# Optimization experiments

Hardware: AMD Instinct MI355X
Metric: run time of the kernel (lower is better)

Reference implementation:

```python
import jax, jax.numpy as jnp
import numpy as np

N_SPK, N_UTT, D_EMB = 1024, 20, 512
COS_EPS = 1e-8   # torch F.cosine_similarity default eps
SIM_EPS = 1e-6   # added to cosine and inside the log, per original code


def setup_inputs() -> dict:
    key = jax.random.key(0)
    embeddings = jax.random.normal(key, (N_SPK, N_UTT, D_EMB), dtype=jnp.float32)
    w = jnp.asarray(10.0, dtype=jnp.float32)
    b = jnp.asarray(-5.0, dtype=jnp.float32)
    return {"embeddings": embeddings, "w": w, "b": b}


def reference(embeddings, w, b):
    N, M, D = embeddings.shape
    sums = embeddings.sum(axis=1)                       # [N, D]
    centroids = sums / M                                # [N, D] full centroids
    cent_excl = (sums[:, None, :] - embeddings) / (M - 1)  # [N, M, D] leave-one-out

    def _norm(x):
        return x / jnp.maximum(jnp.linalg.norm(x, axis=-1, keepdims=True), COS_EPS)

    e_n = _norm(embeddings)          # [N, M, D]
    c_n = _norm(centroids)           # [N, D]
    ce_n = _norm(cent_excl)          # [N, M, D]

    # cosine vs every speaker centroid
    cs = jnp.einsum('nmd,kd->nmk', e_n, c_n)            # [N, M, N]
    # replace same-speaker column with leave-one-out cosine
    diag = jnp.sum(e_n * ce_n, axis=-1)                 # [N, M]
    same = jnp.eye(N, dtype=bool)[:, None, :]           # [N, 1, N]
    cossim = jnp.where(same, diag[:, :, None], cs) + SIM_EPS

    sim = w * cossim + b                                # [N, M, N]
    pos = w * (diag + SIM_EPS) + b                      # sim[j, i, j]
    lse = jnp.log(jnp.sum(jnp.exp(sim), axis=-1) + SIM_EPS)  # [N, M]
    loss = jnp.sum(lse - pos)
    return loss
```

## Files before the change

### kernel.cpp

```cpp
#include <hip/hip_runtime.h>
#include <hip/hip_bf16.h>

typedef unsigned short u16;
typedef unsigned int u32;
typedef __bf16 bf16x8 __attribute__((ext_vector_type(8)));
typedef float f32x4 __attribute__((ext_vector_type(4)));

#define NSPK 1024
#define NUTT 20
#define DEMB 512
#define NROW (NSPK * NUTT)

__device__ __forceinline__ u16 f2bf(float x) {
    union { float f; u32 u; } v; v.f = x;
    u32 r = (v.u + 0x7fffu + ((v.u >> 16) & 1u)) >> 16;
    return (u16)r;
}

__global__ __launch_bounds__(256) void sums_k(const float* __restrict__ E,
                                              float* __restrict__ S,
                                              u16* __restrict__ Bc,
                                              float* __restrict__ ssg,
                                              float* __restrict__ rs,
                                              float* __restrict__ out) {
    __shared__ float s_red[4];
    const int n = blockIdx.x;
    const int t = threadIdx.x;
    const int lane = t & 63, wv = t >> 6;
    const int d0 = t * 2;
    const float* En = E + (size_t)n * (NUTT * DEMB);

    float sx = 0.f, sy = 0.f;
#pragma unroll
    for (int m = 0; m < NUTT; ++m) {
        float2 v = *(const float2*)(En + m * DEMB + d0);
        sx += v.x; sy += v.y;
    }
    *(float2*)(S + (size_t)n * DEMB + d0) = make_float2(sx, sy);

    const float c0 = sx * (1.0f / NUTT), c1 = sy * (1.0f / NUTT);
    float p = c0 * c0 + c1 * c1;
#pragma unroll
    for (int o = 32; o; o >>= 1) p += __shfl_xor(p, o);
    if (lane == 0) s_red[wv] = p;
    __syncthreads();
    p = s_red[0] + s_red[1] + s_red[2] + s_red[3];
    const float rc = 1.0f / fmaxf(sqrtf(p), 1e-8f);
    const u16 cb0 = f2bf(c0 * rc), cb1 = f2bf(c1 * rc);
    *(u32*)(Bc + (size_t)n * DEMB + d0) = (u32)cb0 | ((u32)cb1 << 16);

    if (t == 0) {
        ssg[2 * n + 0] = p * (float)(NUTT * NUTT);
        ssg[2 * n + 1] = rc * (1.0f / NUTT);
    }
    if (t < NUTT) rs[n * NUTT + t] = 0.f;
    if (n == 0 && t == 0) out[0] = 0.f;
}

__global__ __launch_bounds__(256) void rowprep_k(const float* __restrict__ E,
                                                 const float* __restrict__ S,
                                                 const float* __restrict__ ssg,
                                                 u16* __restrict__ A,
                                                 float* __restrict__ diag,
                                                 float* __restrict__ csd) {
    const int lane = threadIdx.x & 63;
    const int r = blockIdx.x * 4 + (threadIdx.x >> 6);
    const int n = r / NUTT;

    const float* e = E + (size_t)r * DEMB + lane * 8;
    const float* s = S + (size_t)n * DEMB + lane * 8;
    const float4 e0 = *(const float4*)(e), e1 = *(const float4*)(e + 4);
    const float4 s0 = *(const float4*)(s), s1 = *(const float4*)(s + 4);

    float ee = e0.x*e0.x + e0.y*e0.y + e0.z*e0.z + e0.w*e0.w
             + e1.x*e1.x + e1.y*e1.y + e1.z*e1.z + e1.w*e1.w;
    float es = e0.x*s0.x + e0.y*s0.y + e0.z*s0.z + e0.w*s0.w
             + e1.x*s1.x + e1.y*s1.y + e1.z*s1.z + e1.w*s1.w;
#pragma unroll
    for (int o = 32; o; o >>= 1) { ee += __shfl_xor(ee, o); es += __shfl_xor(es, o); }

    const float ss = ssg[2 * n + 0], g = ssg[2 * n + 1];
    const float rne = 1.0f / fmaxf(sqrtf(ee), 1e-8f);
    const float pxx = ss - 2.f * es + ee;
    const float dg = (es - ee) * rne / fmaxf(sqrtf(pxx), 1.9e-7f);

    union { u16 h[8]; uint4 q; } pk;
    pk.h[0] = f2bf(e0.x * rne); pk.h[1] = f2bf(e0.y * rne);
    pk.h[2] = f2bf(e0.z * rne); pk.h[3] = f2bf(e0.w * rne);
    pk.h[4] = f2bf(e1.x * rne); pk.h[5] = f2bf(e1.y * rne);
    pk.h[6] = f2bf(e1.z * rne); pk.h[7] = f2bf(e1.w * rne);
    ((uint4*)(A + (size_t)r * DEMB))[lane] = pk.q;

    if (lane == 0) {
        diag[r] = dg;
        csd[r] = es * g * rne;
    }
}

__device__ __forceinline__ void async_copy16(const void* g, void* l) {
    __builtin_amdgcn_global_load_lds(
        (const __attribute__((address_space(1))) void*)g,
        (__attribute__((address_space(3))) void*)l, 16, 0, 0);
}

__global__ __launch_bounds__(256) void gemm_exp(const u16* __restrict__ A,
                                                const u16* __restrict__ Bc,
                                                const float* __restrict__ wp,
                                                const float* __restrict__ bp,
                                                float* __restrict__ rowsum) {
    __shared__ u16 As[128 * 32];
    __shared__ u16 Bs[128 * 32];
    const int t = threadIdx.x;
    const int lane = t & 63, wv = t >> 6;
    const int ml = lane & 15, q = lane >> 4;
    const int wm = wv >> 1, wn = wv & 1;
    const int tileM = blockIdx.x;
    const int tileN = blockIdx.y;

    const float w = *wp, bb = *bp;

    const int c0 = t, c1 = t + 256;
    const int r0 = c0 >> 2, kg0 = (c0 & 3) ^ ((r0 >> 1) & 3);
    const int r1 = c1 >> 2, kg1 = (c1 & 3) ^ ((r1 >> 1) & 3);
    const u16* Ag = A + (size_t)tileM * 128 * DEMB;
    const u16* Bg = Bc + (size_t)tileN * 128 * DEMB;
    u16* as0 = As + c0 * 8; u16* as1 = As + c1 * 8;
    u16* bs0 = Bs + c0 * 8; u16* bs1 = Bs + c1 * 8;

    int ar[4], br[4];
#pragma unroll
    for (int i = 0; i < 4; ++i) {
        int r = wm * 64 + i * 16 + ml;
        ar[i] = r * 32 + ((q ^ ((r >> 1) & 3)) << 3);
        int c = wn * 64 + i * 16 + ml;
        br[i] = c * 32 + ((q ^ ((c >> 1) & 3)) << 3);
    }

    f32x4 acc[4][4];
#pragma unroll
    for (int i = 0; i < 4; ++i)
#pragma unroll
        for (int j = 0; j < 4; ++j) acc[i][j] = (f32x4){0.f, 0.f, 0.f, 0.f};

    for (int kt = 0; kt < DEMB; kt += 32) {
        __syncthreads();
        async_copy16(Ag + (size_t)r0 * DEMB + kt + kg0 * 8, as0);
        async_copy16(Ag + (size_t)r1 * DEMB + kt + kg1 * 8, as1);
        async_copy16(Bg + (size_t)r0 * DEMB + kt + kg0 * 8, bs0);
        async_copy16(Bg + (size_t)r1 * DEMB + kt + kg1 * 8, bs1);
        __syncthreads();

        bf16x8 af[4], bfv[4];
#pragma unroll
        for (int i = 0; i < 4; ++i) af[i] = *(const bf16x8*)(As + ar[i]);
#pragma unroll
        for (int j = 0; j < 4; ++j) bfv[j] = *(const bf16x8*)(Bs + br[j]);
#pragma unroll
        for (int i = 0; i < 4; ++i)
#pragma unroll
            for (int j = 0; j < 4; ++j)
                acc[i][j] = __builtin_amdgcn_mfma_f32_16x16x32_bf16(af[i], bfv[j], acc[i][j], 0, 0, 0);
    }

#pragma unroll
    for (int i = 0; i < 4; ++i) {
        float s0 = 0.f, s1 = 0.f, s2 = 0.f, s3 = 0.f;
#pragma unroll
        for (int j = 0; j < 4; ++j) {
            s0 += __expf(fmaf(w, acc[i][j][0] + 1e-6f, bb));
            s1 += __expf(fmaf(w, acc[i][j][1] + 1e-6f, bb));
            s2 += __expf(fmaf(w, acc[i][j][2] + 1e-6f, bb));
            s3 += __expf(fmaf(w, acc[i][j][3] + 1e-6f, bb));
        }
#pragma unroll
        for (int o = 1; o < 16; o <<= 1) {
            s0 += __shfl_xor(s0, o); s1 += __shfl_xor(s1, o);
            s2 += __shfl_xor(s2, o); s3 += __shfl_xor(s3, o);
        }
        if (ml < 4) {
            float sv = (ml == 0) ? s0 : (ml == 1) ? s1 : (ml == 2) ? s2 : s3;
            int grow = tileM * 128 + wm * 64 + i * 16 + q * 4 + ml;
            atomicAdd(&rowsum[grow], sv);
        }
    }
}

__global__ __launch_bounds__(256) void finalize(const float* __restrict__ rowsum,
                                                const float* __restrict__ diag,
                                                const float* __restrict__ csd,
                                                const float* __restrict__ wp,
                                                const float* __restrict__ bp,
                                                float* __restrict__ out) {
    __shared__ float s_red[4];
    const int r = blockIdx.x * 256 + threadIdx.x;
    const float w = *wp, bb = *bp;
    const float dg = diag[r];
    const float pos = fmaf(w, dg + 1e-6f, bb);
    const float S = rowsum[r] - __expf(fmaf(w, csd[r] + 1e-6f, bb)) + __expf(pos);
    float term = logf(S + 1e-6f) - pos;
    const int lane = threadIdx.x & 63, wv = threadIdx.x >> 6;
#pragma unroll
    for (int o = 32; o; o >>= 1) term += __shfl_xor(term, o);
    if (lane == 0) s_red[wv] = term;
    __syncthreads();
    if (threadIdx.x == 0) atomicAdd(out, s_red[0] + s_red[1] + s_red[2] + s_red[3]);
}

extern "C" void kernel_launch(void* const* d_in, const int* in_sizes, int n_in,
                              void* d_out, int out_size, void* d_ws, size_t ws_size,
                              hipStream_t stream) {
    const float* E = (const float*)d_in[0];
    const float* wp = (const float*)d_in[1];
    const float* bp = (const float*)d_in[2];
    float* out = (float*)d_out;

    char* ws = (char*)d_ws;
    u16* A     = (u16*)(ws);
    u16* Bc    = (u16*)(ws + 20971520);
    float* S   = (float*)(ws + 22020096);
    float* ssg = (float*)(ws + 24117248);
    float* dg  = (float*)(ws + 24125440);
    float* cs  = (float*)(ws + 24207360);
    float* rs  = (float*)(ws + 24289280);

    sums_k<<<NSPK, 256, 0, stream>>>(E, S, Bc, ssg, rs, out);
    rowprep_k<<<5120, 256, 0, stream>>>(E, S, ssg, A, dg, cs);
    gemm_exp<<<dim3(160, 8), 256, 0, stream>>>(A, Bc, wp, bp, rs);
    finalize<<<80, 256, 0, stream>>>(rs, dg, cs, wp, bp, out);
}
```

Measured before the change: 124.9 us.

## Fuse sums and row-prep kernels, double GEMM K-tile to 64

Merges the speaker-sum kernel and the per-row normalisation kernel into one kernel per speaker. Each wave keeps its 5 utterance rows in registers, the four waves reduce their partial sums through LDS, and the same block then emits the centroid bf16, normalised rows, diag and csd. This removes one launch and the second read of the embeddings and of S. Separately, the GEMM K-step grows from 32 to 64 with a wider XOR swizzle, which halves the number of barrier pairs per tile at the cost of more LDS per block.

```diff
diff --git a/kernel.cpp b/kernel.cpp
--- a/kernel.cpp
+++ b/kernel.cpp
@@ -17,84 +17,83 @@
     return (u16)r;
 }
 
-__global__ __launch_bounds__(256) void sums_k(const float* __restrict__ E,
-                                              float* __restrict__ S,
+__global__ __launch_bounds__(256) void prep_f(const float* __restrict__ E,
+                                              u16* __restrict__ A,
                                               u16* __restrict__ Bc,
-                                              float* __restrict__ ssg,
+                                              float* __restrict__ diag,
+                                              float* __restrict__ csd,
                                               float* __restrict__ rs,
                                               float* __restrict__ out) {
-    __shared__ float s_red[4];
+    __shared__ float sbuf[4][DEMB];
+    const int t = threadIdx.x, lane = t & 63, wv = t >> 6;
     const int n = blockIdx.x;
-    const int t = threadIdx.x;
-    const int lane = t & 63, wv = t >> 6;
-    const int d0 = t * 2;
-    const float* En = E + (size_t)n * (NUTT * DEMB);
-
-    float sx = 0.f, sy = 0.f;
-#pragma unroll
-    for (int m = 0; m < NUTT; ++m) {
-        float2 v = *(const float2*)(En + m * DEMB + d0);
-        sx += v.x; sy += v.y;
-    }
-    *(float2*)(S + (size_t)n * DEMB + d0) = make_float2(sx, sy);
-
-    const float c0 = sx * (1.0f / NUTT), c1 = sy * (1.0f / NUTT);
-    float p = c0 * c0 + c1 * c1;
-#pragma unroll
-    for (int o = 32; o; o >>= 1) p += __shfl_xor(p, o);
-    if (lane == 0) s_red[wv] = p;
+    const float* Eb = E + (size_t)n * (NUTT * DEMB) + (size_t)(wv * 5) * DEMB + lane * 8;
+
+    float4 e0[5], e1[5];
+    float4 p0 = {0, 0, 0, 0}, p1 = {0, 0, 0, 0};
+#pragma unroll
+    for (int i = 0; i < 5; ++i) {
+        e0[i] = *(const float4*)(Eb + (size_t)i * DEMB);
+        e1[i] = *(const float4*)(Eb + (size_t)i * DEMB + 4);
+        p0.x += e0[i].x; p0.y += e0[i].y; p0.z += e0[i].z; p0.w += e0[i].w;
+        p1.x += e1[i].x; p1.y += e1[i].y; p1.z += e1[i].z; p1.w += e1[i].w;
+    }
+    *(float4*)(&sbuf[wv][lane * 8])     = p0;
+    *(float4*)(&sbuf[wv][lane * 8 + 4]) = p1;
     __syncthreads();
-    p = s_red[0] + s_red[1] + s_red[2] + s_red[3];
-    const float rc = 1.0f / fmaxf(sqrtf(p), 1e-8f);
-    const u16 cb0 = f2bf(c0 * rc), cb1 = f2bf(c1 * rc);
-    *(u32*)(Bc + (size_t)n * DEMB + d0) = (u32)cb0 | ((u32)cb1 << 16);
-
-    if (t == 0) {
-        ssg[2 * n + 0] = p * (float)(NUTT * NUTT);
-        ssg[2 * n + 1] = rc * (1.0f / NUTT);
-    }
+
+    float4 s0 = {0, 0, 0, 0}, s1 = {0, 0, 0, 0};
+#pragma unroll
+    for (int k = 0; k < 4; ++k) {
+        float4 a = *(const float4*)(&sbuf[k][lane * 8]);
+        float4 b = *(const float4*)(&sbuf[k][lane * 8 + 4]);
+        s0.x += a.x; s0.y += a.y; s0.z += a.z; s0.w += a.w;
+        s1.x += b.x; s1.y += b.y; s1.z += b.z; s1.w += b.w;
+    }
+
+    float ls = s0.x*s0.x + s0.y*s0.y + s0.z*s0.z + s0.w*s0.w
+             + s1.x*s1.x + s1.y*s1.y + s1.z*s1.z + s1.w*s1.w;
+#pragma unroll
+    for (int o = 32; o; o >>= 1) ls += __shfl_xor(ls, o);
+    const float ss = ls;
+    const float rc = 1.0f / fmaxf(sqrtf(ss) * 0.05f, 1e-8f);
+    const float g  = rc * 0.05f;
+
+    union { u16 h[8]; uint4 q; } ck;
+    ck.h[0] = f2bf(s0.x * g); ck.h[1] = f2bf(s0.y * g);
+    ck.h[2] = f2bf(s0.z * g); ck.h[3] = f2bf(s0.w * g);
+    ck.h[4] = f2bf(s1.x * g); ck.h[5] = f2bf(s1.y * g);
+    ck.h[6] = f2bf(s1.z * g); ck.h[7] = f2bf(s1.w * g);
+    ((uint4*)(Bc + (size_t)n * DEMB))[lane] = ck.q;
+
+#pragma unroll
+    for (int i = 0; i < 5; ++i) {
+        float ee = e0[i].x*e0[i].x + e0[i].y*e0[i].y + e0[i].z*e0[i].z + e0[i].w*e0[i].w
+                 + e1[i].x*e1[i].x + e1[i].y*e1[i].y + e1[i].z*e1[i].z + e1[i].w*e1[i].w;
+        float es = e0[i].x*s0.x + e0[i].y*s0.y + e0[i].z*s0.z + e0[i].w*s0.w
+                 + e1[i].x*s1.x + e1[i].y*s1.y + e1[i].z*s1.z + e1[i].w*s1.w;
+#pragma unroll
+        for (int o = 32; o; o >>= 1) { ee += __shfl_xor(ee, o); es += __shfl_xor(es, o); }
+
+        const float rne = 1.0f / fmaxf(sqrtf(ee), 1e-8f);
+        const float pxx = ss - 2.f * es + ee;
+        const float dg  = (es - ee) * rne / fmaxf(sqrtf(pxx), 1.9e-7f);
+
+        const int r = n * NUTT + wv * 5 + i;
+        union { u16 h[8]; uint4 q; } pk;
+        pk.h[0] = f2bf(e0[i].x * rne); pk.h[1] = f2bf(e0[i].y * rne);
+        pk.h[2] = f2bf(e0[i].z * rne); pk.h[3] = f2bf(e0[i].w * rne);
+        pk.h[4] = f2bf(e1[i].x * rne); pk.h[5] = f2bf(e1[i].y * rne);
+        pk.h[6] = f2bf(e1[i].z * rne); pk.h[7] = f2bf(e1[i].w * rne);
+        ((uint4*)(A + (size_t)r * DEMB))[lane] = pk.q;
+        if (lane == 0) {
+            diag[r] = dg;
+            csd[r]  = es * g * rne;
+        }
+    }
+
     if (t < NUTT) rs[n * NUTT + t] = 0.f;
     if (n == 0 && t == 0) out[0] = 0.f;
-}
-
-__global__ __launch_bounds__(256) void rowprep_k(const float* __restrict__ E,
-                                                 const float* __restrict__ S,
-                                                 const float* __restrict__ ssg,
-                                                 u16* __restrict__ A,
-                                                 float* __restrict__ diag,
-                                                 float* __restrict__ csd) {
-    const int lane = threadIdx.x & 63;
-    const int r = blockIdx.x * 4 + (threadIdx.x >> 6);
-    const int n = r / NUTT;
-
-    const float* e = E + (size_t)r * DEMB + lane * 8;
-    const float* s = S + (size_t)n * DEMB + lane * 8;
-    const float4 e0 = *(const float4*)(e), e1 = *(const float4*)(e + 4);
-    const float4 s0 = *(const float4*)(s), s1 = *(const float4*)(s + 4);
-
-    float ee = e0.x*e0.x + e0.y*e0.y + e0.z*e0.z + e0.w*e0.w
-             + e1.x*e1.x + e1.y*e1.y + e1.z*e1.z + e1.w*e1.w;
-    float es = e0.x*s0.x + e0.y*s0.y + e0.z*s0.z + e0.w*s0.w
-             + e1.x*s1.x + e1.y*s1.y + e1.z*s1.z + e1.w*s1.w;
-#pragma unroll
-    for (int o = 32; o; o >>= 1) { ee += __shfl_xor(ee, o); es += __shfl_xor(es, o); }
-
-    const float ss = ssg[2 * n + 0], g = ssg[2 * n + 1];
-    const float rne = 1.0f / fmaxf(sqrtf(ee), 1e-8f);
-    const float pxx = ss - 2.f * es + ee;
-    const float dg = (es - ee) * rne / fmaxf(sqrtf(pxx), 1.9e-7f);
-
-    union { u16 h[8]; uint4 q; } pk;
-    pk.h[0] = f2bf(e0.x * rne); pk.h[1] = f2bf(e0.y * rne);
-    pk.h[2] = f2bf(e0.z * rne); pk.h[3] = f2bf(e0.w * rne);
-    pk.h[4] = f2bf(e1.x * rne); pk.h[5] = f2bf(e1.y * rne);
-    pk.h[6] = f2bf(e1.z * rne); pk.h[7] = f2bf(e1.w * rne);
-    ((uint4*)(A + (size_t)r * DEMB))[lane] = pk.q;
-
-    if (lane == 0) {
-        diag[r] = dg;
-        csd[r] = es * g * rne;
-    }
 }
 
 __device__ __forceinline__ void async_copy16(const void* g, void* l) {
@@ -108,8 +107,8 @@
                                                 const float* __restrict__ wp,
                                                 const float* __restrict__ bp,
                                                 float* __restrict__ rowsum) {
-    __shared__ u16 As[128 * 32];
-    __shared__ u16 Bs[128 * 32];
+    __shared__ u16 As[128 * 64];
+    __shared__ u16 Bs[128 * 64];
     const int t = threadIdx.x;
     const int lane = t & 63, wv = t >> 6;
     const int ml = lane & 15, q = lane >> 4;
@@ -119,21 +118,28 @@
 
     const float w = *wp, bb = *bp;
 
-    const int c0 = t, c1 = t + 256;
-    const int r0 = c0 >> 2, kg0 = (c0 & 3) ^ ((r0 >> 1) & 3);
-    const int r1 = c1 >> 2, kg1 = (c1 & 3) ^ ((r1 >> 1) & 3);
     const u16* Ag = A + (size_t)tileM * 128 * DEMB;
     const u16* Bg = Bc + (size_t)tileN * 128 * DEMB;
-    u16* as0 = As + c0 * 8; u16* as1 = As + c1 * 8;
-    u16* bs0 = Bs + c0 * 8; u16* bs1 = Bs + c1 * 8;
-
-    int ar[4], br[4];
+
+    const u16* asrc[4]; const u16* bsrc[4]; u16* adst[4]; u16* bdst[4];
+#pragma unroll
+    for (int j = 0; j < 4; ++j) {
+        const int c = t + 256 * j;
+        const int r = c >> 3, kg = (c & 7) ^ (r & 7);
+        asrc[j] = Ag + (size_t)r * DEMB + kg * 8;  adst[j] = As + c * 8;
+        bsrc[j] = Bg + (size_t)r * DEMB + kg * 8;  bdst[j] = Bs + c * 8;
+    }
+
+    int aoff[2][4], boff[2][4];
 #pragma unroll
     for (int i = 0; i < 4; ++i) {
-        int r = wm * 64 + i * 16 + ml;
-        ar[i] = r * 32 + ((q ^ ((r >> 1) & 3)) << 3);
-        int c = wn * 64 + i * 16 + ml;
-        br[i] = c * 32 + ((q ^ ((c >> 1) & 3)) << 3);
+        const int r = wm * 64 + i * 16 + ml;
+        const int c = wn * 64 + i * 16 + ml;
+#pragma unroll
+        for (int h = 0; h < 2; ++h) {
+            aoff[h][i] = r * 64 + ((((h << 2) | q) ^ (r & 7)) << 3);
+            boff[h][i] = c * 64 + ((((h << 2) | q) ^ (c & 7)) << 3);
+        }
     }
 
     f32x4 acc[4][4];
@@ -142,24 +148,27 @@
 #pragma unroll
         for (int j = 0; j < 4; ++j) acc[i][j] = (f32x4){0.f, 0.f, 0.f, 0.f};
 
-    for (int kt = 0; kt < DEMB; kt += 32) {
+    for (int kt = 0; kt < DEMB; kt += 64) {
         __syncthreads();
-        async_copy16(Ag + (size_t)r0 * DEMB + kt + kg0 * 8, as0);
-        async_copy16(Ag + (size_t)r1 * DEMB + kt + kg1 * 8, as1);
-        async_copy16(Bg + (size_t)r0 * DEMB + kt + kg0 * 8, bs0);
-        async_copy16(Bg + (size_t)r1 * DEMB + kt + kg1 * 8, bs1);
+#pragma unroll
+        for (int j = 0; j < 4; ++j) async_copy16(asrc[j] + kt, adst[j]);
+#pragma unroll
+        for (int j = 0; j < 4; ++j) async_copy16(bsrc[j] + kt, bdst[j]);
         __syncthreads();
 
-        bf16x8 af[4], bfv[4];
-#pragma unroll
-        for (int i = 0; i < 4; ++i) af[i] = *(const bf16x8*)(As + ar[i]);
-#pragma unroll
-        for (int j = 0; j < 4; ++j) bfv[j] = *(const bf16x8*)(Bs + br[j]);
-#pragma unroll
-        for (int i = 0; i < 4; ++i)
-#pragma unroll
-            for (int j = 0; j < 4; ++j)
-                acc[i][j] = __builtin_amdgcn_mfma_f32_16x16x32_bf16(af[i], bfv[j], acc[i][j], 0, 0, 0);
+#pragma unroll
+        for (int h = 0; h < 2; ++h) {
+            bf16x8 af[4], bfv[4];
+#pragma unroll
+            for (int i = 0; i < 4; ++i) af[i]  = *(const bf16x8*)(As + aoff[h][i]);
+#pragma unroll
+            for (int j = 0; j < 4; ++j) bfv[j] = *(const bf16x8*)(Bs + boff[h][j]);
+#pragma unroll
+            for (int i = 0; i < 4; ++i)
+#pragma unroll
+                for (int j = 0; j < 4; ++j)
+                    acc[i][j] = __builtin_amdgcn_mfma_f32_16x16x32_bf16(af[i], bfv[j], acc[i][j], 0, 0, 0);
+        }
     }
 
 #pragma unroll
@@ -217,14 +226,11 @@
     char* ws = (char*)d_ws;
     u16* A     = (u16*)(ws);
     u16* Bc    = (u16*)(ws + 20971520);
-    float* S   = (float*)(ws + 22020096);
-    float* ssg = (float*)(ws + 24117248);
-    float* dg  = (float*)(ws + 24125440);
-    float* cs  = (float*)(ws + 24207360);
-    float* rs  = (float*)(ws + 24289280);
-
-    sums_k<<<NSPK, 256, 0, stream>>>(E, S, Bc, ssg, rs, out);
-    rowprep_k<<<5120, 256, 0, stream>>>(E, S, ssg, A, dg, cs);
+    float* dg  = (float*)(ws + 22020096);
+    float* cs  = (float*)(ws + 22102016);
+    float* rs  = (float*)(ws + 22183936);
+
+    prep_f<<<NSPK, 256, 0, stream>>>(E, A, Bc, dg, cs, rs, out);
     gemm_exp<<<dim3(160, 8), 256, 0, stream>>>(A, Bc, wp, bp, rs);
     finalize<<<80, 256, 0, stream>>>(rs, dg, cs, wp, bp, out);
 }
```

New measurement: 120.9 us. 3.1% less time.
